# Optimization experiments

Hardware: AMD Instinct MI355X
Metric: run time of the kernel (lower is better)

The kernel has to match this reference:

```python
import jax, jax.numpy as jnp
import numpy as np

EMBED_DIM = 256
NUM_HEADS = 8
PROJ_DIM = EMBED_DIM // NUM_HEADS


def setup_inputs() -> dict:
    key = jax.random.key(0)
    ks = jax.random.split(key, 5)
    scale = 1.0 / np.sqrt(EMBED_DIM)
    inputs = jax.random.normal(ks[0], (2, 12, 12, 12, EMBED_DIM), dtype=jnp.float32)
    Wq = jax.random.normal(ks[1], (EMBED_DIM, EMBED_DIM), dtype=jnp.float32) * scale
    Wk = jax.random.normal(ks[2], (EMBED_DIM, EMBED_DIM), dtype=jnp.float32) * scale
    Wv = jax.random.normal(ks[3], (EMBED_DIM, EMBED_DIM), dtype=jnp.float32) * scale
    Wo = jax.random.normal(ks[4], (EMBED_DIM, EMBED_DIM), dtype=jnp.float32) * scale
    z = jnp.zeros((EMBED_DIM,), dtype=jnp.float32)
    return {"inputs": inputs, "Wq": Wq, "bq": z, "Wk": Wk, "bk": z,
            "Wv": Wv, "bv": z, "Wo": Wo, "bo": z}


def reference(inputs, Wq, bq, Wk, bk, Wv, bv, Wo, bo):
    B, h, w, d, E = inputs.shape
    S = h * w * d  # flattened spatial sequence
    x = inputs.reshape(B, S, E)
    # projections + head split: [B, S, E] -> [B, H, S, P]
    def split_heads(t):
        return t.reshape(B, S, NUM_HEADS, PROJ_DIM).transpose(0, 2, 1, 3)
    q = split_heads(x @ Wq + bq)
    k = split_heads(x @ Wk + bk)
    v = split_heads(x @ Wv + bv)
    # NOTE: original module does NOT scale by 1/sqrt(proj_dim)
    scores = jnp.einsum('bhsp,bhtp->bhst', q, k)  # [B, H, S, S]
    attn = jax.nn.softmax(scores, axis=-1)
    out = jnp.einsum('bhst,bhtp->bhsp', attn, v)  # [B, H, S, P]
    out = out.transpose(0, 2, 1, 3).reshape(B, h, w, d, E)
    return out @ Wo + bo
```

## Files before the change

kernel.cpp:

```cpp
#include <hip/hip_runtime.h>
#include <math.h>

#define EMBED 256
#define HEADS 8
#define PDIM  32
#define BATCH 2
#define SEQ   1728
#define NTOK  (BATCH*SEQ)
#define NE    (NTOK*EMBED)
#define NKT   (SEQ/64)
#define LOG2E 1.44269504088896f

typedef __attribute__((ext_vector_type(8))) __bf16 bf16x8;
typedef __attribute__((ext_vector_type(4))) float  f32x4;
typedef unsigned short ushort_t;
typedef unsigned int   uint_t;

static __device__ __forceinline__ unsigned short f2bf_rne(float f) {
    union { float f; unsigned u; } x; x.f = f;
    unsigned r = x.u + 0x7fffu + ((x.u >> 16) & 1u);
    return (unsigned short)(r >> 16);
}
union v8cast { uint4 u; bf16x8 v; };

static __device__ __forceinline__ void cvt8_hilo(const float f[8], bf16x8& hi, bf16x8& lo) {
    uint4 ph, pl;
    uint_t* phv = (uint_t*)&ph; uint_t* plv = (uint_t*)&pl;
    #pragma unroll
    for (int j = 0; j < 4; ++j) {
        const float f0 = f[2 * j], f1 = f[2 * j + 1];
        const uint_t u0 = __float_as_uint(f0) + 0x8000u;
        const uint_t u1 = __float_as_uint(f1) + 0x8000u;
        phv[j] = __builtin_amdgcn_perm(u1, u0, 0x07060302u);
        const float l0 = f0 - __uint_as_float(u0 & 0xFFFF0000u);
        const float l1 = f1 - __uint_as_float(u1 & 0xFFFF0000u);
        plv[j] = __builtin_amdgcn_perm(__float_as_uint(l1) + 0x8000u,
                                       __float_as_uint(l0) + 0x8000u, 0x07060302u);
    }
    v8cast ch; ch.u = ph; hi = ch.v;
    v8cast cl; cl.u = pl; lo = cl.v;
}

__global__ __launch_bounds__(64) void qkv_gemm_kernel(
    const float* __restrict__ x,
    const float* __restrict__ Wq, const float* __restrict__ bq,
    const float* __restrict__ Wk, const float* __restrict__ bk,
    const float* __restrict__ Wv, const float* __restrict__ bv,
    ushort_t* __restrict__ qo, ushort_t* __restrict__ ko, ushort_t* __restrict__ vt)
{
    const int lane = threadIdx.x, li = lane & 15, quad = lane >> 4;
    const int m0 = blockIdx.x * 64, n0 = blockIdx.y * 32, z = blockIdx.z;
    const float* __restrict__ W    = (z == 0) ? Wq : (z == 1) ? Wk : Wv;
    const float* __restrict__ bias = (z == 0) ? bq : (z == 1) ? bk : bv;

    const float* ap = x + (size_t)(m0 + li) * EMBED + quad * 8;

    f32x4 acc[4][2];
    #pragma unroll
    for (int mt = 0; mt < 4; ++mt)
        #pragma unroll
        for (int nt = 0; nt < 2; ++nt)
            acc[mt][nt] = (f32x4){0.f, 0.f, 0.f, 0.f};

    #pragma unroll 2
    for (int k0 = 0; k0 < EMBED; k0 += 32) {
        bf16x8 ah[4], al[4];
        #pragma unroll
        for (int mt = 0; mt < 4; ++mt) {
            float af[8];
            *(float4*)&af[0] = *(const float4*)(ap + (size_t)mt * 16 * EMBED + k0);
            *(float4*)&af[4] = *(const float4*)(ap + (size_t)mt * 16 * EMBED + k0 + 4);
            cvt8_hilo(af, ah[mt], al[mt]);
        }
        bf16x8 bh[2], bl[2];
        #pragma unroll
        for (int nt = 0; nt < 2; ++nt) {
            const int n = n0 + nt * 16 + li;
            const float* wp = W + (size_t)(k0 + quad * 8) * EMBED + n;
            float bf[8];
            #pragma unroll
            for (int jj = 0; jj < 8; ++jj) bf[jj] = wp[(size_t)jj * EMBED];
            cvt8_hilo(bf, bh[nt], bl[nt]);
        }
        #pragma unroll
        for (int mt = 0; mt < 4; ++mt)
            #pragma unroll
            for (int nt = 0; nt < 2; ++nt) {
                acc[mt][nt] = __builtin_amdgcn_mfma_f32_16x16x32_bf16(ah[mt], bh[nt], acc[mt][nt], 0, 0, 0);
                acc[mt][nt] = __builtin_amdgcn_mfma_f32_16x16x32_bf16(al[mt], bh[nt], acc[mt][nt], 0, 0, 0);
                acc[mt][nt] = __builtin_amdgcn_mfma_f32_16x16x32_bf16(ah[mt], bl[nt], acc[mt][nt], 0, 0, 0);
            }
    }

    const int b = m0 / SEQ;
    const int sbase = m0 - b * SEQ;

    if (z <= 1) {
        ushort_t* __restrict__ dst = z ? ko : qo;
        #pragma unroll
        for (int nt = 0; nt < 2; ++nt) {
            const int gcol = n0 + nt * 16 + li;
            const int h = gcol >> 5, p = gcol & 31;
            const float bb = bias[gcol];
            ushort_t* base = dst + ((size_t)(b * HEADS + h) * SEQ) * PDIM + p;
            #pragma unroll
            for (int mt = 0; mt < 4; ++mt)
                #pragma unroll
                for (int r = 0; r < 4; ++r) {
                    const int s = sbase + mt * 16 + quad * 4 + r;
                    base[(size_t)s * PDIM] = f2bf_rne(acc[mt][nt][r] + bb);
                }
        }
    } else {
        #pragma unroll
        for (int nt = 0; nt < 2; ++nt) {
            const int gcol = n0 + nt * 16 + li;
            const int h = gcol >> 5, p = gcol & 31;
            const float bb = bias[gcol];
            ushort_t* base = vt + ((size_t)(b * HEADS + h) * PDIM + p) * SEQ;
            #pragma unroll
            for (int mt = 0; mt < 4; ++mt) {
                const int s0 = sbase + mt * 16 + quad * 4;
                ushort4 w;
                w.x = f2bf_rne(acc[mt][nt][0] + bb);
                w.y = f2bf_rne(acc[mt][nt][1] + bb);
                w.z = f2bf_rne(acc[mt][nt][2] + bb);
                w.w = f2bf_rne(acc[mt][nt][3] + bb);
                *(ushort4*)&base[s0] = w;
            }
        }
    }
}

__global__ __launch_bounds__(256) void attn_kernel(
    const ushort_t* __restrict__ q, const ushort_t* __restrict__ k,
    const ushort_t* __restrict__ vt, ushort_t* __restrict__ aob)
{
    const int t    = threadIdx.x;
    const int lane = t & 63;
    const int w    = t >> 6;
    const int li   = lane & 15;
    const int quad = lane >> 4;
    const int bh = blockIdx.y;
    const int b  = bh >> 3, h = bh & 7;
    const int q0 = blockIdx.x * 64 + w * 16;

    const ushort_t* __restrict__ qb = q  + (size_t)bh * SEQ * PDIM;
    const ushort_t* __restrict__ kb = k  + (size_t)bh * SEQ * PDIM;
    const ushort_t* __restrict__ vb = vt + (size_t)bh * PDIM * SEQ;

    __shared__ ushort_t Ks[2][64][40];
    __shared__ ushort_t Vs[2][32][72];
    __shared__ ushort_t Ps[4][16][72];

    const bf16x8 qfrag = *(const bf16x8*)(qb + (size_t)(q0 + li) * PDIM + quad * 8);

    const int jk = w * 16 + (lane >> 2), ck = (lane & 3) * 8;
    const int pv = w * 8 + (lane >> 3),  cv = (lane & 7) * 8;
    const ushort_t* kgp = kb + (size_t)jk * PDIM + ck;
    const ushort_t* vgp = vb + (size_t)pv * SEQ + cv;

    f32x4 o0 = {0.f, 0.f, 0.f, 0.f};
    f32x4 o1 = {0.f, 0.f, 0.f, 0.f};
    float m_run = -__builtin_inff(), l_run = 0.f;

    uint4 kreg = *(const uint4*)(kgp);
    uint4 vreg = *(const uint4*)(vgp);

    for (int kt = 0; kt < NKT; ++kt) {
        const int p = kt & 1;
        *(uint4*)&Ks[p][jk][ck] = kreg;
        *(uint4*)&Vs[p][pv][cv] = vreg;
        __syncthreads();
        if (kt + 1 < NKT) {
            kreg = *(const uint4*)(kgp + (size_t)(kt + 1) * 64 * PDIM);
            vreg = *(const uint4*)(vgp + (kt + 1) * 64);
        }

        const f32x4 zero = {0.f, 0.f, 0.f, 0.f};
        f32x4 st[4];
        #pragma unroll
        for (int jt = 0; jt < 4; ++jt) {
            const bf16x8 kf = *(const bf16x8*)&Ks[p][jt * 16 + li][quad * 8];
            st[jt] = __builtin_amdgcn_mfma_f32_16x16x32_bf16(kf, qfrag, zero, 0, 0, 0);
        }

        float tm = st[0][0];
        #pragma unroll
        for (int jt = 0; jt < 4; ++jt)
            #pragma unroll
            for (int r = 0; r < 4; ++r) tm = fmaxf(tm, st[jt][r]);
        tm = fmaxf(tm, __shfl_xor(tm, 16));
        tm = fmaxf(tm, __shfl_xor(tm, 32));
        const float mnew  = fmaxf(m_run, tm);
        const float negml = -(mnew * LOG2E);

        float ps = 0.f;
        #pragma unroll
        for (int jt = 0; jt < 4; ++jt) {
            const float p0 = __builtin_amdgcn_exp2f(fmaf(st[jt][0], LOG2E, negml));
            const float p1 = __builtin_amdgcn_exp2f(fmaf(st[jt][1], LOG2E, negml));
            const float p2 = __builtin_amdgcn_exp2f(fmaf(st[jt][2], LOG2E, negml));
            const float p3 = __builtin_amdgcn_exp2f(fmaf(st[jt][3], LOG2E, negml));
            ps += (p0 + p1) + (p2 + p3);
            uint2 pw;
            pw.x = __builtin_amdgcn_perm(__float_as_uint(p1) + 0x8000u,
                                         __float_as_uint(p0) + 0x8000u, 0x07060302u);
            pw.y = __builtin_amdgcn_perm(__float_as_uint(p3) + 0x8000u,
                                         __float_as_uint(p2) + 0x8000u, 0x07060302u);
            *(uint2*)&Ps[w][li][16 * jt + 4 * quad] = pw;
        }
        ps += __shfl_xor(ps, 16);
        ps += __shfl_xor(ps, 32);

        const float alpha = __builtin_amdgcn_exp2f(fmaf(m_run, LOG2E, negml));
        l_run = fmaf(l_run, alpha, ps);
        m_run = mnew;

        float af[4];
        #pragma unroll
        for (int r = 0; r < 4; ++r) af[r] = __shfl(alpha, 4 * quad + r);
        #pragma unroll
        for (int r = 0; r < 4; ++r) { o0[r] *= af[r]; o1[r] *= af[r]; }

        const bf16x8 pa0 = *(const bf16x8*)&Ps[w][li][8 * quad];
        const bf16x8 pa1 = *(const bf16x8*)&Ps[w][li][32 + 8 * quad];
        const bf16x8 vf00 = *(const bf16x8*)&Vs[p][li][quad * 8];
        const bf16x8 vf01 = *(const bf16x8*)&Vs[p][16 + li][quad * 8];
        const bf16x8 vf10 = *(const bf16x8*)&Vs[p][li][32 + quad * 8];
        const bf16x8 vf11 = *(const bf16x8*)&Vs[p][16 + li][32 + quad * 8];
        o0 = __builtin_amdgcn_mfma_f32_16x16x32_bf16(pa0, vf00, o0, 0, 0, 0);
        o0 = __builtin_amdgcn_mfma_f32_16x16x32_bf16(pa1, vf10, o0, 0, 0, 0);
        o1 = __builtin_amdgcn_mfma_f32_16x16x32_bf16(pa0, vf01, o1, 0, 0, 0);
        o1 = __builtin_amdgcn_mfma_f32_16x16x32_bf16(pa1, vf11, o1, 0, 0, 0);
    }

    float linv[4];
    #pragma unroll
    for (int r = 0; r < 4; ++r) linv[r] = 1.0f / __shfl(l_run, 4 * quad + r);
    #pragma unroll
    for (int r = 0; r < 4; ++r) {
        const int s = q0 + 4 * quad + r;
        ushort_t* row = aob + ((size_t)(b * SEQ + s)) * EMBED + h * PDIM;
        row[li]      = f2bf_rne(o0[r] * linv[r]);
        row[16 + li] = f2bf_rne(o1[r] * linv[r]);
    }
}

__global__ __launch_bounds__(64) void out_gemm_kernel(
    const ushort_t* __restrict__ a, const float* __restrict__ Wo,
    const float* __restrict__ bo, float* __restrict__ out)
{
    const int lane = threadIdx.x, li = lane & 15, quad = lane >> 4;
    const int m0 = blockIdx.x * 64, n0 = blockIdx.y * 16;

    const ushort_t* aph = a + (size_t)(m0 + li) * EMBED + quad * 8;

    f32x4 acc[4];
    #pragma unroll
    for (int mt = 0; mt < 4; ++mt) acc[mt] = (f32x4){0.f, 0.f, 0.f, 0.f};

    #pragma unroll 2
    for (int k0 = 0; k0 < EMBED; k0 += 32) {
        bf16x8 ah[4];
        #pragma unroll
        for (int mt = 0; mt < 4; ++mt)
            ah[mt] = *(const bf16x8*)(aph + (size_t)mt * 16 * EMBED + k0);
        const float* wp = Wo + (size_t)(k0 + quad * 8) * EMBED + n0 + li;
        uint4 pb;
        uint_t* pbv = (uint_t*)&pb;
        #pragma unroll
        for (int j = 0; j < 4; ++j) {
            const uint_t u0 = __float_as_uint(wp[(size_t)(2 * j) * EMBED])     + 0x8000u;
            const uint_t u1 = __float_as_uint(wp[(size_t)(2 * j + 1) * EMBED]) + 0x8000u;
            pbv[j] = __builtin_amdgcn_perm(u1, u0, 0x07060302u);
        }
        v8cast cb; cb.u = pb;
        #pragma unroll
        for (int mt = 0; mt < 4; ++mt)
            acc[mt] = __builtin_amdgcn_mfma_f32_16x16x32_bf16(ah[mt], cb.v, acc[mt], 0, 0, 0);
    }

    const float bb = bo[n0 + li];
    #pragma unroll
    for (int mt = 0; mt < 4; ++mt)
        #pragma unroll
        for (int r = 0; r < 4; ++r) {
            const int row = m0 + mt * 16 + quad * 4 + r;
            out[(size_t)row * EMBED + n0 + li] = acc[mt][r] + bb;
        }
}

extern "C" void kernel_launch(void* const* d_in, const int* in_sizes, int n_in,
                              void* d_out, int out_size, void* d_ws, size_t ws_size,
                              hipStream_t stream)
{
    const float* x  = (const float*)d_in[0];
    const float* Wq = (const float*)d_in[1];
    const float* bq = (const float*)d_in[2];
    const float* Wk = (const float*)d_in[3];
    const float* bk = (const float*)d_in[4];
    const float* Wv = (const float*)d_in[5];
    const float* bv = (const float*)d_in[6];
    const float* Wo = (const float*)d_in[7];
    const float* bo = (const float*)d_in[8];
    float* out = (float*)d_out;

    ushort_t* ws  = (ushort_t*)d_ws;
    ushort_t* qb  = ws;
    ushort_t* kb  = qb + (size_t)NE;
    ushort_t* vt  = kb + (size_t)NE;
    ushort_t* aob = vt + (size_t)NE;

    qkv_gemm_kernel<<<dim3(NTOK / 64, 8, 3), 64, 0, stream>>>(
        x, Wq, bq, Wk, bk, Wv, bv, qb, kb, vt);
    attn_kernel<<<dim3(SEQ / 64, BATCH * HEADS), 256, 0, stream>>>(qb, kb, vt, aob);
    out_gemm_kernel<<<dim3(NTOK / 64, 16), 64, 0, stream>>>(aob, Wo, bo, out);
}
```

Baseline: 119.9 us.

## Widen attention KV tiles to 128 keys with a 64-key tail and remap blocks

```diff
diff --git a/kernel.cpp b/kernel.cpp
--- a/kernel.cpp
+++ b/kernel.cpp
@@ -8,7 +8,9 @@
 #define SEQ   1728
 #define NTOK  (BATCH*SEQ)
 #define NE    (NTOK*EMBED)
-#define NKT   (SEQ/64)
+#define KVB   128
+#define NMAIN 13
+#define TAIL0 1664
 #define LOG2E 1.44269504088896f
 
 typedef __attribute__((ext_vector_type(8))) __bf16 bf16x8;
@@ -141,41 +143,122 @@
     const int w    = t >> 6;
     const int li   = lane & 15;
     const int quad = lane >> 4;
-    const int bh = blockIdx.y;
+    const int bid = blockIdx.x;
+    const int g = bid & 7, j = bid >> 3;
+    const int bh = g * 2 + (j >= 27 ? 1 : 0);
+    const int qt = (j >= 27) ? (j - 27) : j;
     const int b  = bh >> 3, h = bh & 7;
-    const int q0 = blockIdx.x * 64 + w * 16;
+    const int q0 = qt * 64 + w * 16;
 
     const ushort_t* __restrict__ qb = q  + (size_t)bh * SEQ * PDIM;
     const ushort_t* __restrict__ kb = k  + (size_t)bh * SEQ * PDIM;
     const ushort_t* __restrict__ vb = vt + (size_t)bh * PDIM * SEQ;
 
-    __shared__ ushort_t Ks[2][64][40];
-    __shared__ ushort_t Vs[2][32][72];
-    __shared__ ushort_t Ps[4][16][72];
+    __shared__ ushort_t Ks[2][128][40];
+    __shared__ ushort_t Vs[2][32][136];
+    __shared__ ushort_t Ps[4][16][136];
 
     const bf16x8 qfrag = *(const bf16x8*)(qb + (size_t)(q0 + li) * PDIM + quad * 8);
 
-    const int jk = w * 16 + (lane >> 2), ck = (lane & 3) * 8;
-    const int pv = w * 8 + (lane >> 3),  cv = (lane & 7) * 8;
-    const ushort_t* kgp = kb + (size_t)jk * PDIM + ck;
-    const ushort_t* vgp = vb + (size_t)pv * SEQ + cv;
+    const int krow = t >> 1, kcol = (t & 1) * 16;
+    const int vrow = t >> 3, vkey = (t & 7) * 16;
+    const ushort_t* kgp = kb + (size_t)krow * PDIM + kcol;
+    const ushort_t* vgp = vb + (size_t)vrow * SEQ + vkey;
 
     f32x4 o0 = {0.f, 0.f, 0.f, 0.f};
     f32x4 o1 = {0.f, 0.f, 0.f, 0.f};
     float m_run = -__builtin_inff(), l_run = 0.f;
 
-    uint4 kreg = *(const uint4*)(kgp);
-    uint4 vreg = *(const uint4*)(vgp);
-
-    for (int kt = 0; kt < NKT; ++kt) {
-        const int p = kt & 1;
-        *(uint4*)&Ks[p][jk][ck] = kreg;
-        *(uint4*)&Vs[p][pv][cv] = vreg;
+    uint4 ka  = *(const uint4*)(kgp);
+    uint4 kc  = *(const uint4*)(kgp + 8);
+    uint4 va  = *(const uint4*)(vgp);
+    uint4 vc  = *(const uint4*)(vgp + 8);
+
+    for (int it = 0; it < NMAIN; ++it) {
+        const int p = it & 1;
+        *(uint4*)&Ks[p][krow][kcol]     = ka;
+        *(uint4*)&Ks[p][krow][kcol + 8] = kc;
+        *(uint4*)&Vs[p][vrow][vkey]     = va;
+        *(uint4*)&Vs[p][vrow][vkey + 8] = vc;
         __syncthreads();
-        if (kt + 1 < NKT) {
-            kreg = *(const uint4*)(kgp + (size_t)(kt + 1) * 64 * PDIM);
-            vreg = *(const uint4*)(vgp + (kt + 1) * 64);
-        }
+        if (it + 1 < NMAIN) {
+            const size_t ko = (size_t)(it + 1) * KVB * PDIM;
+            ka = *(const uint4*)(kgp + ko);
+            kc = *(const uint4*)(kgp + ko + 8);
+            va = *(const uint4*)(vgp + (it + 1) * KVB);
+            vc = *(const uint4*)(vgp + (it + 1) * KVB + 8);
+        } else {
+            const ushort_t* kt_ = kb + (size_t)(TAIL0 + (krow & 63)) * PDIM + kcol;
+            ka = *(const uint4*)(kt_);
+            kc = *(const uint4*)(kt_ + 8);
+            const ushort_t* vt_ = vb + (size_t)vrow * SEQ + TAIL0 + (vkey & 63);
+            va = *(const uint4*)(vt_);
+            vc = *(const uint4*)(vt_ + 8);
+        }
+
+        const f32x4 zero = {0.f, 0.f, 0.f, 0.f};
+        f32x4 st[8];
+        #pragma unroll
+        for (int jt = 0; jt < 8; ++jt) {
+            const bf16x8 kf = *(const bf16x8*)&Ks[p][jt * 16 + li][quad * 8];
+            st[jt] = __builtin_amdgcn_mfma_f32_16x16x32_bf16(kf, qfrag, zero, 0, 0, 0);
+        }
+
+        float tm = st[0][0];
+        #pragma unroll
+        for (int jt = 0; jt < 8; ++jt)
+            #pragma unroll
+            for (int r = 0; r < 4; ++r) tm = fmaxf(tm, st[jt][r]);
+        tm = fmaxf(tm, __shfl_xor(tm, 16));
+        tm = fmaxf(tm, __shfl_xor(tm, 32));
+        const float mnew  = fmaxf(m_run, tm);
+        const float negml = -(mnew * LOG2E);
+
+        float ps = 0.f;
+        #pragma unroll
+        for (int jt = 0; jt < 8; ++jt) {
+            const float p0 = __builtin_amdgcn_exp2f(fmaf(st[jt][0], LOG2E, negml));
+            const float p1 = __builtin_amdgcn_exp2f(fmaf(st[jt][1], LOG2E, negml));
+            const float p2 = __builtin_amdgcn_exp2f(fmaf(st[jt][2], LOG2E, negml));
+            const float p3 = __builtin_amdgcn_exp2f(fmaf(st[jt][3], LOG2E, negml));
+            ps += (p0 + p1) + (p2 + p3);
+            uint2 pw;
+            pw.x = __builtin_amdgcn_perm(__float_as_uint(p1) + 0x8000u,
+                                         __float_as_uint(p0) + 0x8000u, 0x07060302u);
+            pw.y = __builtin_amdgcn_perm(__float_as_uint(p3) + 0x8000u,
+                                         __float_as_uint(p2) + 0x8000u, 0x07060302u);
+            *(uint2*)&Ps[w][li][16 * jt + 4 * quad] = pw;
+        }
+        ps += __shfl_xor(ps, 16);
+        ps += __shfl_xor(ps, 32);
+
+        const float alpha = __builtin_amdgcn_exp2f(fmaf(m_run, LOG2E, negml));
+        l_run = fmaf(l_run, alpha, ps);
+        m_run = mnew;
+
+        float af[4];
+        #pragma unroll
+        for (int r = 0; r < 4; ++r) af[r] = __shfl(alpha, 4 * quad + r);
+        #pragma unroll
+        for (int r = 0; r < 4; ++r) { o0[r] *= af[r]; o1[r] *= af[r]; }
+
+        #pragma unroll
+        for (int c = 0; c < 4; ++c) {
+            const bf16x8 pa  = *(const bf16x8*)&Ps[w][li][32 * c + 8 * quad];
+            const bf16x8 vf0 = *(const bf16x8*)&Vs[p][li][32 * c + quad * 8];
+            const bf16x8 vf1 = *(const bf16x8*)&Vs[p][16 + li][32 * c + quad * 8];
+            o0 = __builtin_amdgcn_mfma_f32_16x16x32_bf16(pa, vf0, o0, 0, 0, 0);
+            o1 = __builtin_amdgcn_mfma_f32_16x16x32_bf16(pa, vf1, o1, 0, 0, 0);
+        }
+    }
+
+    {
+        const int p = NMAIN & 1;
+        *(uint4*)&Ks[p][krow][kcol]     = ka;
+        *(uint4*)&Ks[p][krow][kcol + 8] = kc;
+        *(uint4*)&Vs[p][vrow][vkey]     = va;
+        *(uint4*)&Vs[p][vrow][vkey + 8] = vc;
+        __syncthreads();
 
         const f32x4 zero = {0.f, 0.f, 0.f, 0.f};
         f32x4 st[4];
@@ -223,16 +306,14 @@
         #pragma unroll
         for (int r = 0; r < 4; ++r) { o0[r] *= af[r]; o1[r] *= af[r]; }
 
-        const bf16x8 pa0 = *(const bf16x8*)&Ps[w][li][8 * quad];
-        const bf16x8 pa1 = *(const bf16x8*)&Ps[w][li][32 + 8 * quad];
-        const bf16x8 vf00 = *(const bf16x8*)&Vs[p][li][quad * 8];
-        const bf16x8 vf01 = *(const bf16x8*)&Vs[p][16 + li][quad * 8];
-        const bf16x8 vf10 = *(const bf16x8*)&Vs[p][li][32 + quad * 8];
-        const bf16x8 vf11 = *(const bf16x8*)&Vs[p][16 + li][32 + quad * 8];
-        o0 = __builtin_amdgcn_mfma_f32_16x16x32_bf16(pa0, vf00, o0, 0, 0, 0);
-        o0 = __builtin_amdgcn_mfma_f32_16x16x32_bf16(pa1, vf10, o0, 0, 0, 0);
-        o1 = __builtin_amdgcn_mfma_f32_16x16x32_bf16(pa0, vf01, o1, 0, 0, 0);
-        o1 = __builtin_amdgcn_mfma_f32_16x16x32_bf16(pa1, vf11, o1, 0, 0, 0);
+        #pragma unroll
+        for (int c = 0; c < 2; ++c) {
+            const bf16x8 pa  = *(const bf16x8*)&Ps[w][li][32 * c + 8 * quad];
+            const bf16x8 vf0 = *(const bf16x8*)&Vs[p][li][32 * c + quad * 8];
+            const bf16x8 vf1 = *(const bf16x8*)&Vs[p][16 + li][32 * c + quad * 8];
+            o0 = __builtin_amdgcn_mfma_f32_16x16x32_bf16(pa, vf0, o0, 0, 0, 0);
+            o1 = __builtin_amdgcn_mfma_f32_16x16x32_bf16(pa, vf1, o1, 0, 0, 0);
+        }
     }
 
     float linv[4];
@@ -314,6 +395,6 @@
 
     qkv_gemm_kernel<<<dim3(NTOK / 64, 8, 3), 64, 0, stream>>>(
         x, Wq, bq, Wk, bk, Wv, bv, qb, kb, vt);
-    attn_kernel<<<dim3(SEQ / 64, BATCH * HEADS), 256, 0, stream>>>(qb, kb, vt, aob);
+    attn_kernel<<<dim3(432), 256, 0, stream>>>(qb, kb, vt, aob);
     out_gemm_kernel<<<dim3(NTOK / 64, 16), 64, 0, stream>>>(aob, Wo, bo, out);
 }
```

New measurement: 119.5 us. About the same (-0.3%).
